# Performance work log

Measured on AMD Instinct MI355X. Metric: run time of the kernel, lower is better.

The kernel has to match this reference:

```python
import jax, jax.numpy as jnp
import numpy as np
from jax.scipy.special import logsumexp

# config (matches init_kwargs)
D_IN, D_OUT = 768, 256
P = 2
BLUR = 0.5
SCALING = 0.8
SCALING_FACTOR = 1.0
N_ITERS = 36  # fixed-length eps schedule (clamped at blur), jit-friendly


def setup_inputs() -> dict:
    key = jax.random.key(0)
    k1, k2, k3, k4 = jax.random.split(key, 4)
    d = jax.random.normal(k1, (4096, D_IN), dtype=jnp.float32)
    s1 = jax.random.normal(k2, (1024, D_IN), dtype=jnp.float32)
    s2 = jax.random.normal(k3, (1024, D_IN), dtype=jnp.float32)
    # learned projection parameter (scaled init so projected coords are O(1))
    M = jax.random.normal(k4, (D_IN, D_OUT), dtype=jnp.float32) / np.sqrt(D_IN)
    return {"d": d, "s1": s1, "s2": s2, "M": M}


def _sq_cost(u, v):
    # C[i,j] = ||u_i - v_j||^2 / 2  (geomloss p=2 cost)
    sq = (jnp.sum(u * u, -1)[:, None] + jnp.sum(v * v, -1)[None, :]
          - 2.0 * (u @ v.T))
    return jnp.maximum(sq, 0.0) * 0.5


def _softmin(eps, C, h):
    # -eps * log sum_j exp(h_j - C_ij/eps)   -> shape [C.shape[0]]
    return -eps * logsumexp(h[None, :] - C / eps, axis=1)


def _sinkhorn_divergence(x, y):
    n, m = x.shape[0], y.shape[0]
    a_log = jnp.full((n,), -np.log(n), dtype=x.dtype)  # uniform log-weights
    b_log = jnp.full((m,), -np.log(m), dtype=x.dtype)

    C_xy = _sq_cost(x, y)   # [n, m]
    C_xx = _sq_cost(x, x)   # [n, n]  (debiasing term)
    C_yy = _sq_cost(y, y)   # [m, m]

    # bounding-box diameter of the joint cloud (no grad, like geomloss)
    z = jax.lax.stop_gradient(jnp.concatenate([x, y], axis=0))
    diam = jnp.sqrt(jnp.sum((z.max(0) - z.min(0)) ** 2)) + 1e-6

    # eps-scaling schedule: scale from diameter down to blur, eps = scale^p
    scales = jnp.maximum(BLUR, diam * (SCALING ** jnp.arange(N_ITERS, dtype=x.dtype)))
    eps_list = scales ** P
    eps0 = eps_list[0]
    eps_f = jnp.asarray(BLUR ** P, dtype=x.dtype)

    # init potentials at the largest eps
    f_aa = _softmin(eps0, C_xx, a_log)
    g_bb = _softmin(eps0, C_yy, b_log)
    f_ab = _softmin(eps0, C_xy, b_log)
    g_ab = _softmin(eps0, C_xy.T, a_log)

    @jax.checkpoint
    def step(carry, eps):
        f_aa, g_bb, f_ab, g_ab = carry
        # simultaneous (Jacobi) updates, symmetrized by averaging
        ft = _softmin(eps, C_xy, b_log + g_ab / eps)
        gt = _softmin(eps, C_xy.T, a_log + f_ab / eps)
        f_aa = 0.5 * (f_aa + _softmin(eps, C_xx, a_log + f_aa / eps))
        g_bb = 0.5 * (g_bb + _softmin(eps, C_yy, b_log + g_bb / eps))
        f_ab = 0.5 * (f_ab + ft)
        g_ab = 0.5 * (g_ab + gt)
        return (f_aa, g_bb, f_ab, g_ab), None

    (f_aa, g_bb, f_ab, g_ab), _ = jax.lax.scan(
        step, (f_aa, g_bb, f_ab, g_ab), eps_list)

    # final non-averaged extrapolation at eps = blur^p
    f_ab_n = _softmin(eps_f, C_xy, b_log + g_ab / eps_f)
    g_ab_n = _softmin(eps_f, C_xy.T, a_log + f_ab / eps_f)
    f_aa_n = _softmin(eps_f, C_xx, a_log + f_aa / eps_f)
    g_bb_n = _softmin(eps_f, C_yy, b_log + g_bb / eps_f)

    # debiased divergence with uniform weights: <a, f_ab - f_aa> + <b, g_ab - g_bb>
    return jnp.mean(f_ab_n - f_aa_n) + jnp.mean(g_ab_n - g_bb_n)


def reference(d, s1, s2, M):
    xd = d @ M
    x1 = s1 @ M
    x2 = s2 @ M
    dist1 = _sinkhorn_divergence(xd, x1)
    dist2 = _sinkhorn_divergence(xd, x2)
    return jax.nn.sigmoid(SCALING_FACTOR * (dist2 - dist1))
```

## Files before the change

### kernel.cpp

```cpp
#include <hip/hip_runtime.h>
#include <hip/hip_bf16.h>
#include <math.h>

using ull = unsigned long long;
typedef unsigned short u16x8 __attribute__((ext_vector_type(8)));
typedef __attribute__((ext_vector_type(8))) short bf16x8;
typedef __attribute__((ext_vector_type(4))) float f32x4;

#define ND 4096ull
#define NS 1024ull
#define DOUT 256ull
#define DIN 768ull
#define NIT 36

constexpr ull U_CXX = 0;
constexpr ull U_CXY = U_CXX + ND*ND;
constexpr ull U_CYX = U_CXY + 2*ND*NS;
constexpr ull U_CYY = U_CYX + 2*ND*NS;
constexpr ull U_TOT = U_CYY + 2*NS*NS;
constexpr ull P_XDH = U_TOT;
constexpr ull P_XDM = P_XDH + ND*DOUT;
constexpr ull P_X1H = P_XDM + ND*DOUT;
constexpr ull P_X1M = P_X1H + NS*DOUT;
constexpr ull P_X2H = P_X1M + NS*DOUT;
constexpr ull P_X2M = P_X2H + NS*DOUT;
constexpr ull P_DH  = P_X2M + NS*DOUT;
constexpr ull P_DM  = P_DH + ND*DIN;
constexpr ull P_S1H = P_DM + ND*DIN;
constexpr ull P_S1M = P_S1H + NS*DIN;
constexpr ull P_S2H = P_S1M + NS*DIN;
constexpr ull P_S2M = P_S2H + NS*DIN;
constexpr ull P_MTH = P_S2M + NS*DIN;
constexpr ull P_MTM = P_MTH + DOUT*DIN;
constexpr ull U_END = P_MTM + DOUT*DIN;

constexpr ull O_XD   = U_END / 2;
constexpr ull O_X1   = O_XD + ND*DOUT;
constexpr ull O_X2   = O_X1 + NS*DOUT;
constexpr ull O_MT   = O_X2 + NS*DOUT;
constexpr ull O_ND_  = O_MT + DOUT*DIN;
constexpr ull O_N1   = O_ND_ + ND;
constexpr ull O_N2   = O_N1 + NS;
constexpr ull O_FAB  = O_N2 + NS;
constexpr ull O_GAB  = O_FAB + 4*ND;
constexpr ull O_FAA  = O_GAB + 4*NS;
constexpr ull O_GBB  = O_FAA + 4*ND;
constexpr ull O_FABN = O_GBB + 4*NS;
constexpr ull O_GABN = O_FABN + 2*ND;
constexpr ull O_FAAN = O_GABN + 2*NS;
constexpr ull O_GBBN = O_FAAN + 2*ND;
constexpr ull O_EPS  = O_GBBN + 2*NS;
constexpr ull O_QS   = O_EPS + 2*NIT;
constexpr ull O_DIST = O_QS + 2;
constexpr ull WS_FLOATS = O_DIST + 2;
constexpr ull O_PMIN = O_MT;
constexpr ull O_PMAX = O_MT + 96*256;

constexpr float LOG2E = 1.4426950408889634f;
constexpr float LN2   = 0.69314718055994531f;
constexpr float A_LOG2 = -12.0f;
constexpr float B_LOG2 = -10.0f;

__device__ __forceinline__ float wave_max(float v) {
    #pragma unroll
    for (int o = 32; o; o >>= 1) v = fmaxf(v, __shfl_xor(v, o));
    return v;
}
__device__ __forceinline__ float wave_sum(float v) {
    #pragma unroll
    for (int o = 32; o; o >>= 1) v += __shfl_xor(v, o);
    return v;
}

__device__ __forceinline__ unsigned short f2bf_rn(float x) {
    union { float f; unsigned u; } v; v.f = x;
    const unsigned r = v.u + 0x7FFFu + ((v.u >> 16) & 1u);
    return (unsigned short)(r >> 16);
}
__device__ __forceinline__ float bf2f(unsigned short b) {
    union { unsigned u; float f; } v; v.u = ((unsigned)b) << 16; return v.f;
}

__global__ __launch_bounds__(256)
void transpose_M_k(const float* __restrict__ M, float* __restrict__ Mt)
{
    int idx = blockIdx.x * 256 + threadIdx.x;
    int r = idx >> 8;
    int c = idx & 255;
    Mt[(size_t)c * DIN + r] = M[idx];
}

__global__ __launch_bounds__(256)
void pack_bf16_gen(const float* __restrict__ X,
                   unsigned short* __restrict__ Phi, unsigned short* __restrict__ Pmi,
                   int KB)
{
    const int p = blockIdx.x;
    const int t = threadIdx.x;
    const int K = KB * 32;
    for (int s = t; s < KB * 64; s += 256) {
        const int kb = s >> 6, l = s & 63;
        const int row = p * 16 + (l & 15);
        const int k0 = kb * 32 + ((l >> 4) << 3);
        const float* src = X + (ull)row * K + k0;
        u16x8 hi, mi;
        #pragma unroll
        for (int e = 0; e < 8; e++) {
            const float x = src[e];
            const unsigned short h = f2bf_rn(x);
            hi[e] = h;
            mi[e] = f2bf_rn(x - bf2f(h));
        }
        const ull o = (((ull)p * KB + kb) * 64 + l) * 8;
        *(u16x8*)&Phi[o] = hi;
        *(u16x8*)&Pmi[o] = mi;
    }
}

__global__ __launch_bounds__(256)
void gemm_proj_mfma(const unsigned short* __restrict__ Ahi, const unsigned short* __restrict__ Ami,
                    const unsigned short* __restrict__ Bhi, const unsigned short* __restrict__ Bmi,
                    float* __restrict__ C, int N, int KB)
{
    const int l = threadIdx.x & 63;
    const int w = threadIdx.x >> 6;
    const int n0 = blockIdx.x * 64, m0 = blockIdx.y * 128;
    const int pA0 = (m0 >> 4) + w * 2;
    const int pB0 = n0 >> 4;
    f32x4 acc[2][4] = {};
    for (int kb = 0; kb < KB; kb++) {
        const ull a0o = (((ull)(pA0 + 0) * KB + kb) * 64 + l) * 8;
        const ull a1o = (((ull)(pA0 + 1) * KB + kb) * 64 + l) * 8;
        const bf16x8 aH0 = *(const bf16x8*)&Ahi[a0o];
        const bf16x8 aM0 = *(const bf16x8*)&Ami[a0o];
        const bf16x8 aH1 = *(const bf16x8*)&Ahi[a1o];
        const bf16x8 aM1 = *(const bf16x8*)&Ami[a1o];
        #pragma unroll
        for (int j = 0; j < 4; j++) {
            const ull bo = (((ull)(pB0 + j) * KB + kb) * 64 + l) * 8;
            const bf16x8 bH = *(const bf16x8*)&Bhi[bo];
            const bf16x8 bM = *(const bf16x8*)&Bmi[bo];
            acc[0][j] = __builtin_amdgcn_mfma_f32_16x16x32_bf16(aH0, bH, acc[0][j], 0, 0, 0);
            acc[0][j] = __builtin_amdgcn_mfma_f32_16x16x32_bf16(aH0, bM, acc[0][j], 0, 0, 0);
            acc[0][j] = __builtin_amdgcn_mfma_f32_16x16x32_bf16(aM0, bH, acc[0][j], 0, 0, 0);
            acc[1][j] = __builtin_amdgcn_mfma_f32_16x16x32_bf16(aH1, bH, acc[1][j], 0, 0, 0);
            acc[1][j] = __builtin_amdgcn_mfma_f32_16x16x32_bf16(aH1, bM, acc[1][j], 0, 0, 0);
            acc[1][j] = __builtin_amdgcn_mfma_f32_16x16x32_bf16(aM1, bH, acc[1][j], 0, 0, 0);
        }
    }
    const int col = l & 15;
    #pragma unroll
    for (int i = 0; i < 2; i++) {
        const int row0 = m0 + w * 32 + i * 16 + ((l >> 4) << 2);
        #pragma unroll
        for (int r = 0; r < 4; r++) {
            const ull rowb = (ull)(row0 + r) * N + n0;
            #pragma unroll
            for (int j = 0; j < 4; j++)
                C[rowb + j * 16 + col] = acc[i][j][r];
        }
    }
}

__device__ __forceinline__ unsigned int quant16(float c, float s) {
    return __float2uint_rn(fminf(c * s, 65535.0f));
}

__global__ __launch_bounds__(256)
void gemm_cost_mfma(const unsigned short* __restrict__ Ahi, const unsigned short* __restrict__ Ami,
                    const unsigned short* __restrict__ Bhi, const unsigned short* __restrict__ Bmi,
                    unsigned short* __restrict__ C,
                    const float* __restrict__ na, const float* __restrict__ nb,
                    const float* __restrict__ qsp, int N)
{
    const int l = threadIdx.x & 63;
    const int w = threadIdx.x >> 6;
    const int n0 = blockIdx.x * 64, m0 = blockIdx.y * 128;
    const int pA0 = (m0 >> 4) + w * 2;
    const int pB0 = n0 >> 4;
    f32x4 acc[2][4] = {};
    #pragma unroll
    for (int kb = 0; kb < 8; kb++) {
        const ull a0o = (((ull)(pA0 + 0) * 8 + kb) * 64 + l) * 8;
        const ull a1o = (((ull)(pA0 + 1) * 8 + kb) * 64 + l) * 8;
        const bf16x8 aH0 = *(const bf16x8*)&Ahi[a0o];
        const bf16x8 aM0 = *(const bf16x8*)&Ami[a0o];
        const bf16x8 aH1 = *(const bf16x8*)&Ahi[a1o];
        const bf16x8 aM1 = *(const bf16x8*)&Ami[a1o];
        #pragma unroll
        for (int j = 0; j < 4; j++) {
            const ull bo = (((ull)(pB0 + j) * 8 + kb) * 64 + l) * 8;
            const bf16x8 bH = *(const bf16x8*)&Bhi[bo];
            const bf16x8 bM = *(const bf16x8*)&Bmi[bo];
            acc[0][j] = __builtin_amdgcn_mfma_f32_16x16x32_bf16(aH0, bH, acc[0][j], 0, 0, 0);
            acc[0][j] = __builtin_amdgcn_mfma_f32_16x16x32_bf16(aH0, bM, acc[0][j], 0, 0, 0);
            acc[0][j] = __builtin_amdgcn_mfma_f32_16x16x32_bf16(aM0, bH, acc[0][j], 0, 0, 0);
            acc[1][j] = __builtin_amdgcn_mfma_f32_16x16x32_bf16(aH1, bH, acc[1][j], 0, 0, 0);
            acc[1][j] = __builtin_amdgcn_mfma_f32_16x16x32_bf16(aH1, bM, acc[1][j], 0, 0, 0);
            acc[1][j] = __builtin_amdgcn_mfma_f32_16x16x32_bf16(aM1, bH, acc[1][j], 0, 0, 0);
        }
    }
    const float s = qsp[0];
    const int col = l & 15;
    float nbj[4];
    #pragma unroll
    for (int j = 0; j < 4; j++) nbj[j] = nb[n0 + j * 16 + col];
    #pragma unroll
    for (int i = 0; i < 2; i++) {
        const int row0 = m0 + w * 32 + i * 16 + ((l >> 4) << 2);
        #pragma unroll
        for (int r = 0; r < 4; r++) {
            const float nar = na[row0 + r];
            const ull rowb = (ull)(row0 + r) * N + n0;
            #pragma unroll
            for (int j = 0; j < 4; j++)
                C[rowb + j * 16 + col] =
                    (unsigned short)quant16(0.5f * fmaxf(nar + nbj[j] - 2.0f * acc[i][j][r], 0.0f), s);
        }
    }
}

__global__ __launch_bounds__(256)
void row_norm(const float* __restrict__ x, float* __restrict__ o)
{
    const int i = blockIdx.x;
    const float v = x[(size_t)i * DOUT + threadIdx.x];
    float s = wave_sum(v * v);
    __shared__ float red[4];
    const int wid = threadIdx.x >> 6, lane = threadIdx.x & 63;
    if (lane == 0) red[wid] = s;
    __syncthreads();
    if (threadIdx.x == 0) o[i] = red[0] + red[1] + red[2] + red[3];
}

__global__ __launch_bounds__(256)
void colminmax_k(const float* __restrict__ xd, const float* __restrict__ x1,
                 const float* __restrict__ x2, float* __restrict__ ws)
{
    const int b = blockIdx.x, c = threadIdx.x;
    const float* src; int r0;
    if (b < 64)      { src = xd; r0 = b * 64; }
    else if (b < 80) { src = x1; r0 = (b - 64) * 64; }
    else             { src = x2; r0 = (b - 80) * 64; }
    float mn = 3.4e38f, mx = -3.4e38f;
    for (int r = 0; r < 64; r++) {
        const float v = src[(size_t)(r0 + r) * DOUT + c];
        mn = fminf(mn, v); mx = fmaxf(mx, v);
    }
    ws[O_PMIN + (ull)b * 256 + c] = mn;
    ws[O_PMAX + (ull)b * 256 + c] = mx;
}

__global__ __launch_bounds__(256)
void eps_k(float* __restrict__ ws)
{
    const int c = threadIdx.x;
    const float* pmin = ws + O_PMIN;
    const float* pmax = ws + O_PMAX;
    float mnd = 3.4e38f, mxd = -3.4e38f;
    float mn1 = 3.4e38f, mx1 = -3.4e38f;
    float mn2 = 3.4e38f, mx2 = -3.4e38f;
    for (int b = 0;  b < 64; b++) { mnd = fminf(mnd, pmin[b*256+c]); mxd = fmaxf(mxd, pmax[b*256+c]); }
    for (int b = 64; b < 80; b++) { mn1 = fminf(mn1, pmin[b*256+c]); mx1 = fmaxf(mx1, pmax[b*256+c]); }
    for (int b = 80; b < 96; b++) { mn2 = fminf(mn2, pmin[b*256+c]); mx2 = fmaxf(mx2, pmax[b*256+c]); }
    const float d1 = fmaxf(mxd, mx1) - fminf(mnd, mn1);
    const float d2 = fmaxf(mxd, mx2) - fminf(mnd, mn2);
    float s1 = wave_sum(d1 * d1);
    float s2 = wave_sum(d2 * d2);
    __shared__ float r1[4], r2[4];
    const int wid = c >> 6, lane = c & 63;
    if (lane == 0) { r1[wid] = s1; r2[wid] = s2; }
    __syncthreads();
    if (c == 0) {
        const float d1s = r1[0]+r1[1]+r1[2]+r1[3];
        const float d2s = r2[0]+r2[1]+r2[2]+r2[3];
        const float cb = 0.5f * fmaxf(d1s, d2s) * 1.02f + 1.0f;
        ws[O_QS]     = 65535.0f / cb;
        ws[O_QS + 1] = cb / 65535.0f;
    }
    if (c < 2 * NIT) {
        const int div = c / NIT, tt = c % NIT;
        const float ss = div ? (r2[0]+r2[1]+r2[2]+r2[3]) : (r1[0]+r1[1]+r1[2]+r1[3]);
        const float diam = sqrtf(ss) + 1e-6f;
        const float sc = fmaxf(0.5f, diam * powf(0.8f, (float)tt));
        ws[O_EPS + (ull)div * NIT + tt] = sc * sc;
    }
}

template<int NC>
__device__ __forceinline__ void softmin_row_q(
    const unsigned short* __restrict__ Crow, const float* __restrict__ hvec,
    float hc2, float eps, float qs,
    const float* __restrict__ selfv, float* __restrict__ outp,
    int row, int phase, int lane)
{
    const float ie2 = LOG2E / eps;
    const float qsc = -qs * ie2;
    const u16x8* Q8 = (const u16x8*)Crow;
    const float4* H4 = (const float4*)hvec;
    float v[NC * 8];
    #pragma unroll
    for (int c = 0; c < NC; c++) {
        const u16x8 q = Q8[c * 64 + lane];
        if (hvec) {
            const float4 ha = H4[c * 128 + lane * 2];
            const float4 hb = H4[c * 128 + lane * 2 + 1];
            const float hv[8] = {ha.x, ha.y, ha.z, ha.w, hb.x, hb.y, hb.z, hb.w};
            #pragma unroll
            for (int e = 0; e < 8; e++)
                v[c*8 + e] = fmaf((float)q[e], qsc, fmaf(hv[e], ie2, hc2));
        } else {
            #pragma unroll
            for (int e = 0; e < 8; e++)
                v[c*8 + e] = fmaf((float)q[e], qsc, hc2);
        }
    }
    float m = v[0];
    #pragma unroll
    for (int k = 1; k < NC * 8; k++) m = fmaxf(m, v[k]);
    m = wave_max(m);
    float s = 0.0f;
    #pragma unroll
    for (int k = 0; k < NC * 8; k++) s += exp2f(v[k] - m);
    s = wave_sum(s);
    if (lane == 0) {
        float res = -eps * LN2 * (m + log2f(s));
        if (phase == 1) res = 0.5f * (selfv[row] + res);
        outp[row] = res;
    }
}

__global__ __launch_bounds__(256)
void sinkhorn_phase(float* __restrict__ ws, int phase, int t)
{
    const unsigned short* uq = (const unsigned short*)ws;
    const int wid = threadIdx.x >> 6, lane = threadIdx.x & 63;
    const int w = blockIdx.x * 4 + wid;
    const float qs = ws[O_QS + 1];
    int rb, wb;
    if (phase == 0) { rb = 0; wb = 0; }
    else { rb = t & 1; wb = rb ^ 1; }

    if (w < 8192) {
        const int div = w >> 12, i = w & 4095;
        const float eps = (phase == 2) ? 0.25f : ws[O_EPS + (ull)div * NIT + t];
        const unsigned short* Crow = uq + U_CXY + (ull)div * ND * NS + (ull)i * NS;
        const float* gab_r = ws + O_GAB + ((ull)div * 2 + rb) * NS;
        const float* fab_r = ws + O_FAB + ((ull)div * 2 + rb) * ND;
        float* outp = (phase == 2) ? (ws + O_FABN + (ull)div * ND)
                                   : (ws + O_FAB + ((ull)div * 2 + wb) * ND);
        softmin_row_q<2>(Crow, phase ? gab_r : nullptr, B_LOG2, eps, qs, fab_r, outp, i, phase, lane);
    } else if (w < 10240) {
        const int q = w - 8192, div = q >> 10, j = q & 1023;
        const float eps = (phase == 2) ? 0.25f : ws[O_EPS + (ull)div * NIT + t];
        const unsigned short* Crow = uq + U_CYX + (ull)div * ND * NS + (ull)j * ND;
        const float* fab_r = ws + O_FAB + ((ull)div * 2 + rb) * ND;
        const float* gab_r = ws + O_GAB + ((ull)div * 2 + rb) * NS;
        float* outp = (phase == 2) ? (ws + O_GABN + (ull)div * NS)
                                   : (ws + O_GAB + ((ull)div * 2 + wb) * NS);
        softmin_row_q<8>(Crow, phase ? fab_r : nullptr, A_LOG2, eps, qs, gab_r, outp, j, phase, lane);
    } else if (w < 14336) {
        const int i = w - 10240;
        const float eps0 = (phase == 2) ? 0.25f : ws[O_EPS + t];
        const float eps1 = (phase == 2) ? 0.25f : ws[O_EPS + NIT + t];
        const unsigned short* Crow = uq + U_CXX + (ull)i * ND;
        const float* faa_r0 = ws + O_FAA + (ull)rb * ND;
        const float* faa_r1 = ws + O_FAA + (2ull + rb) * ND;
        float* out0 = (phase == 2) ? (ws + O_FAAN)      : (ws + O_FAA + (ull)wb * ND);
        float* out1 = (phase == 2) ? (ws + O_FAAN + ND) : (ws + O_FAA + (2ull + wb) * ND);
        softmin_row_q<8>(Crow, phase ? faa_r0 : nullptr, A_LOG2, eps0, qs, faa_r0, out0, i, phase, lane);
        softmin_row_q<8>(Crow, phase ? faa_r1 : nullptr, A_LOG2, eps1, qs, faa_r1, out1, i, phase, lane);
    } else {
        const int q = w - 14336, div = q >> 10, i = q & 1023;
        const float eps = (phase == 2) ? 0.25f : ws[O_EPS + (ull)div * NIT + t];
        const unsigned short* Crow = uq + U_CYY + (ull)div * NS * NS + (ull)i * NS;
        const float* gbb_r = ws + O_GBB + ((ull)div * 2 + rb) * NS;
        float* outp = (phase == 2) ? (ws + O_GBBN + (ull)div * NS)
                                   : (ws + O_GBB + ((ull)div * 2 + wb) * NS);
        softmin_row_q<2>(Crow, phase ? gbb_r : nullptr, B_LOG2, eps, qs, gbb_r, outp, i, phase, lane);
    }
}

__global__ __launch_bounds__(256)
void reduce_dist(float* __restrict__ ws)
{
    const int d = blockIdx.x;
    const int tix = threadIdx.x;
    float s = 0.0f;
    #pragma unroll
    for (int k = 0; k < 16; k++) {
        const int i = tix + k * 256;
        s += (ws[O_FABN + (ull)d * ND + i] - ws[O_FAAN + (ull)d * ND + i]) * (1.0f / 4096.0f);
    }
    #pragma unroll
    for (int k = 0; k < 4; k++) {
        const int j = tix + k * 256;
        s += (ws[O_GABN + (ull)d * NS + j] - ws[O_GBBN + (ull)d * NS + j]) * (1.0f / 1024.0f);
    }
    s = wave_sum(s);
    __shared__ float red[4];
    const int wid = tix >> 6, lane = tix & 63;
    if (lane == 0) red[wid] = s;
    __syncthreads();
    if (tix == 0) ws[O_DIST + d] = red[0] + red[1] + red[2] + red[3];
}

__global__ void finalize_k(const float* __restrict__ ws, float* __restrict__ out)
{
    const float x = ws[O_DIST + 1] - ws[O_DIST + 0];
    out[0] = 1.0f / (1.0f + expf(-x));
}

extern "C" void kernel_launch(void* const* d_in, const int* in_sizes, int n_in,
                              void* d_out, int out_size, void* d_ws, size_t ws_size,
                              hipStream_t stream)
{
    if (ws_size < WS_FLOATS * sizeof(float)) return;

    const float* dmat = (const float*)d_in[0];
    const float* s1   = (const float*)d_in[1];
    const float* s2   = (const float*)d_in[2];
    const float* M    = (const float*)d_in[3];
    float* ws  = (float*)d_ws;
    float* out = (float*)d_out;
    unsigned short* uq = (unsigned short*)d_ws;

    float* Mt = ws + O_MT;
    float* xd = ws + O_XD;
    float* x1 = ws + O_X1;
    float* x2 = ws + O_X2;

    transpose_M_k<<<768, 256, 0, stream>>>(M, Mt);
    pack_bf16_gen<<<256, 256, 0, stream>>>(dmat, uq + P_DH,  uq + P_DM,  24);
    pack_bf16_gen<<<64,  256, 0, stream>>>(s1,   uq + P_S1H, uq + P_S1M, 24);
    pack_bf16_gen<<<64,  256, 0, stream>>>(s2,   uq + P_S2H, uq + P_S2M, 24);
    pack_bf16_gen<<<16,  256, 0, stream>>>(Mt,   uq + P_MTH, uq + P_MTM, 24);
    gemm_proj_mfma<<<dim3(4, 32), 256, 0, stream>>>(uq+P_DH,  uq+P_DM,  uq+P_MTH, uq+P_MTM, xd, 256, 24);
    gemm_proj_mfma<<<dim3(4, 8),  256, 0, stream>>>(uq+P_S1H, uq+P_S1M, uq+P_MTH, uq+P_MTM, x1, 256, 24);
    gemm_proj_mfma<<<dim3(4, 8),  256, 0, stream>>>(uq+P_S2H, uq+P_S2M, uq+P_MTH, uq+P_MTM, x2, 256, 24);
    row_norm<<<4096, 256, 0, stream>>>(xd, ws + O_ND_);
    row_norm<<<1024, 256, 0, stream>>>(x1, ws + O_N1);
    row_norm<<<1024, 256, 0, stream>>>(x2, ws + O_N2);
    colminmax_k<<<96, 256, 0, stream>>>(xd, x1, x2, ws);
    eps_k<<<1, 256, 0, stream>>>(ws);
    pack_bf16_gen<<<256, 256, 0, stream>>>(xd, uq + P_XDH, uq + P_XDM, 8);
    pack_bf16_gen<<<64,  256, 0, stream>>>(x1, uq + P_X1H, uq + P_X1M, 8);
    pack_bf16_gen<<<64,  256, 0, stream>>>(x2, uq + P_X2H, uq + P_X2M, 8);
    const float* qsp = ws + O_QS;
    const float* nd_ = ws + O_ND_;
    const float* n1  = ws + O_N1;
    const float* n2  = ws + O_N2;
    gemm_cost_mfma<<<dim3(64, 32), 256, 0, stream>>>(uq+P_XDH, uq+P_XDM, uq+P_XDH, uq+P_XDM, uq + U_CXX,         nd_, nd_, qsp, 4096);
    gemm_cost_mfma<<<dim3(16, 32), 256, 0, stream>>>(uq+P_XDH, uq+P_XDM, uq+P_X1H, uq+P_X1M, uq + U_CXY,         nd_, n1,  qsp, 1024);
    gemm_cost_mfma<<<dim3(64, 8),  256, 0, stream>>>(uq+P_X1H, uq+P_X1M, uq+P_XDH, uq+P_XDM, uq + U_CYX,         n1,  nd_, qsp, 4096);
    gemm_cost_mfma<<<dim3(16, 32), 256, 0, stream>>>(uq+P_XDH, uq+P_XDM, uq+P_X2H, uq+P_X2M, uq + U_CXY + ND*NS, nd_, n2,  qsp, 1024);
    gemm_cost_mfma<<<dim3(64, 8),  256, 0, stream>>>(uq+P_X2H, uq+P_X2M, uq+P_XDH, uq+P_XDM, uq + U_CYX + ND*NS, n2,  nd_, qsp, 4096);
    gemm_cost_mfma<<<dim3(16, 8),  256, 0, stream>>>(uq+P_X1H, uq+P_X1M, uq+P_X1H, uq+P_X1M, uq + U_CYY,         n1,  n1,  qsp, 1024);
    gemm_cost_mfma<<<dim3(16, 8),  256, 0, stream>>>(uq+P_X2H, uq+P_X2M, uq+P_X2H, uq+P_X2M, uq + U_CYY + NS*NS, n2,  n2,  qsp, 1024);
    sinkhorn_phase<<<4096, 256, 0, stream>>>(ws, 0, 0);
    for (int t = 0; t < NIT; t++)
        sinkhorn_phase<<<4096, 256, 0, stream>>>(ws, 1, t);
    sinkhorn_phase<<<4096, 256, 0, stream>>>(ws, 2, 36);
    reduce_dist<<<2, 256, 0, stream>>>(ws);
    finalize_k<<<1, 1, 0, stream>>>(ws, out);
}
```

Measured before the change: 1.431 ms.

## Split long softmin rows across block waves with shared-memory logsumexp merge

Each Sinkhorn softmin row of length 4096 (the C_yx and C_xx rows) is now split into four 1024-element segments, one per wave in a block. The partial max and sum from each wave are merged in shared memory. The C_xx work for the two divergences now runs in separate blocks instead of one wave doing both, and the grid grows from 4096 to 12800 blocks, so every wave handles the same amount of work. This is meant to remove the long-tail imbalance and short the serial per-wave chain. In exchange it adds a block barrier, and each C_xx row is read twice (once per divergence), which relies on the cache to hold it.

```diff
diff --git a/kernel.cpp b/kernel.cpp
--- a/kernel.cpp
+++ b/kernel.cpp
@@ -287,24 +287,18 @@
     }
 }
 
-template<int NC>
-__device__ __forceinline__ void softmin_row_q(
-    const unsigned short* __restrict__ Crow, const float* __restrict__ hvec,
-    float hc2, float eps, float qs,
-    const float* __restrict__ selfv, float* __restrict__ outp,
-    int row, int phase, int lane)
-{
-    const float ie2 = LOG2E / eps;
-    const float qsc = -qs * ie2;
-    const u16x8* Q8 = (const u16x8*)Crow;
-    const float4* H4 = (const float4*)hvec;
-    float v[NC * 8];
-    #pragma unroll
-    for (int c = 0; c < NC; c++) {
-        const u16x8 q = Q8[c * 64 + lane];
-        if (hvec) {
-            const float4 ha = H4[c * 128 + lane * 2];
-            const float4 hb = H4[c * 128 + lane * 2 + 1];
+__device__ __forceinline__ void softmin_1k(
+    const unsigned short* __restrict__ Cseg, const float* __restrict__ hseg,
+    float hc2, float ie2, float qsc, int lane, float& mO, float& sO)
+{
+    float v[16];
+    #pragma unroll
+    for (int c = 0; c < 2; c++) {
+        const int off = c * 512 + lane * 8;
+        const u16x8 q = *(const u16x8*)&Cseg[off];
+        if (hseg) {
+            const float4 ha = *(const float4*)&hseg[off];
+            const float4 hb = *(const float4*)&hseg[off + 4];
             const float hv[8] = {ha.x, ha.y, ha.z, ha.w, hb.x, hb.y, hb.z, hb.w};
             #pragma unroll
             for (int e = 0; e < 8; e++)
@@ -317,67 +311,102 @@
     }
     float m = v[0];
     #pragma unroll
-    for (int k = 1; k < NC * 8; k++) m = fmaxf(m, v[k]);
+    for (int k = 1; k < 16; k++) m = fmaxf(m, v[k]);
     m = wave_max(m);
     float s = 0.0f;
     #pragma unroll
-    for (int k = 0; k < NC * 8; k++) s += exp2f(v[k] - m);
-    s = wave_sum(s);
-    if (lane == 0) {
-        float res = -eps * LN2 * (m + log2f(s));
-        if (phase == 1) res = 0.5f * (selfv[row] + res);
-        outp[row] = res;
-    }
+    for (int k = 0; k < 16; k++) s += exp2f(v[k] - m);
+    sO = wave_sum(s);
+    mO = m;
 }
 
 __global__ __launch_bounds__(256)
 void sinkhorn_phase(float* __restrict__ ws, int phase, int t)
 {
+    __shared__ float mS[4], sS[4];
     const unsigned short* uq = (const unsigned short*)ws;
     const int wid = threadIdx.x >> 6, lane = threadIdx.x & 63;
-    const int w = blockIdx.x * 4 + wid;
     const float qs = ws[O_QS + 1];
     int rb, wb;
     if (phase == 0) { rb = 0; wb = 0; }
     else { rb = t & 1; wb = rb ^ 1; }
-
-    if (w < 8192) {
-        const int div = w >> 12, i = w & 4095;
+    const int b = blockIdx.x;
+
+    if (b < 2048) {
+        const int div = b >> 10;
+        const int i = ((b & 1023) << 2) + wid;
         const float eps = (phase == 2) ? 0.25f : ws[O_EPS + (ull)div * NIT + t];
+        const float ie2 = LOG2E / eps, qsc = -qs * ie2;
         const unsigned short* Crow = uq + U_CXY + (ull)div * ND * NS + (ull)i * NS;
-        const float* gab_r = ws + O_GAB + ((ull)div * 2 + rb) * NS;
-        const float* fab_r = ws + O_FAB + ((ull)div * 2 + rb) * ND;
+        const float* h    = phase ? (ws + O_GAB + ((ull)div * 2 + rb) * NS) : nullptr;
+        const float* self = ws + O_FAB + ((ull)div * 2 + rb) * ND;
         float* outp = (phase == 2) ? (ws + O_FABN + (ull)div * ND)
                                    : (ws + O_FAB + ((ull)div * 2 + wb) * ND);
-        softmin_row_q<2>(Crow, phase ? gab_r : nullptr, B_LOG2, eps, qs, fab_r, outp, i, phase, lane);
-    } else if (w < 10240) {
-        const int q = w - 8192, div = q >> 10, j = q & 1023;
+        float m, s;
+        softmin_1k(Crow, h, B_LOG2, ie2, qsc, lane, m, s);
+        if (lane == 0) {
+            float res = -eps * LN2 * (m + log2f(s));
+            if (phase == 1) res = 0.5f * (self[i] + res);
+            outp[i] = res;
+        }
+    } else if (b < 4096) {
+        const int q = b - 2048, div = q >> 10, j = q & 1023;
         const float eps = (phase == 2) ? 0.25f : ws[O_EPS + (ull)div * NIT + t];
-        const unsigned short* Crow = uq + U_CYX + (ull)div * ND * NS + (ull)j * ND;
-        const float* fab_r = ws + O_FAB + ((ull)div * 2 + rb) * ND;
-        const float* gab_r = ws + O_GAB + ((ull)div * 2 + rb) * NS;
+        const float ie2 = LOG2E / eps, qsc = -qs * ie2;
+        const unsigned short* Cseg = uq + U_CYX + (ull)div * ND * NS + (ull)j * ND + wid * 1024;
+        const float* h    = phase ? (ws + O_FAB + ((ull)div * 2 + rb) * ND + wid * 1024) : nullptr;
+        const float* self = ws + O_GAB + ((ull)div * 2 + rb) * NS;
         float* outp = (phase == 2) ? (ws + O_GABN + (ull)div * NS)
                                    : (ws + O_GAB + ((ull)div * 2 + wb) * NS);
-        softmin_row_q<8>(Crow, phase ? fab_r : nullptr, A_LOG2, eps, qs, gab_r, outp, j, phase, lane);
-    } else if (w < 14336) {
-        const int i = w - 10240;
-        const float eps0 = (phase == 2) ? 0.25f : ws[O_EPS + t];
-        const float eps1 = (phase == 2) ? 0.25f : ws[O_EPS + NIT + t];
-        const unsigned short* Crow = uq + U_CXX + (ull)i * ND;
-        const float* faa_r0 = ws + O_FAA + (ull)rb * ND;
-        const float* faa_r1 = ws + O_FAA + (2ull + rb) * ND;
-        float* out0 = (phase == 2) ? (ws + O_FAAN)      : (ws + O_FAA + (ull)wb * ND);
-        float* out1 = (phase == 2) ? (ws + O_FAAN + ND) : (ws + O_FAA + (2ull + wb) * ND);
-        softmin_row_q<8>(Crow, phase ? faa_r0 : nullptr, A_LOG2, eps0, qs, faa_r0, out0, i, phase, lane);
-        softmin_row_q<8>(Crow, phase ? faa_r1 : nullptr, A_LOG2, eps1, qs, faa_r1, out1, i, phase, lane);
+        float m, s;
+        softmin_1k(Cseg, h, A_LOG2, ie2, qsc, lane, m, s);
+        if (lane == 0) { mS[wid] = m; sS[wid] = s; }
+        __syncthreads();
+        if (threadIdx.x == 0) {
+            const float m0 = fmaxf(fmaxf(mS[0], mS[1]), fmaxf(mS[2], mS[3]));
+            const float st = sS[0]*exp2f(mS[0]-m0) + sS[1]*exp2f(mS[1]-m0)
+                           + sS[2]*exp2f(mS[2]-m0) + sS[3]*exp2f(mS[3]-m0);
+            float res = -eps * LN2 * (m0 + log2f(st));
+            if (phase == 1) res = 0.5f * (self[j] + res);
+            outp[j] = res;
+        }
+    } else if (b < 12288) {
+        const int q = b - 4096, div = q >> 12, i = q & 4095;
+        const float eps = (phase == 2) ? 0.25f : ws[O_EPS + (ull)div * NIT + t];
+        const float ie2 = LOG2E / eps, qsc = -qs * ie2;
+        const unsigned short* Cseg = uq + U_CXX + (ull)i * ND + wid * 1024;
+        const float* hbase = ws + O_FAA + ((ull)div * 2 + rb) * ND;
+        const float* h = phase ? (hbase + wid * 1024) : nullptr;
+        float* outp = (phase == 2) ? (ws + O_FAAN + (ull)div * ND)
+                                   : (ws + O_FAA + ((ull)div * 2 + wb) * ND);
+        float m, s;
+        softmin_1k(Cseg, h, A_LOG2, ie2, qsc, lane, m, s);
+        if (lane == 0) { mS[wid] = m; sS[wid] = s; }
+        __syncthreads();
+        if (threadIdx.x == 0) {
+            const float m0 = fmaxf(fmaxf(mS[0], mS[1]), fmaxf(mS[2], mS[3]));
+            const float st = sS[0]*exp2f(mS[0]-m0) + sS[1]*exp2f(mS[1]-m0)
+                           + sS[2]*exp2f(mS[2]-m0) + sS[3]*exp2f(mS[3]-m0);
+            float res = -eps * LN2 * (m0 + log2f(st));
+            if (phase == 1) res = 0.5f * (hbase[i] + res);
+            outp[i] = res;
+        }
     } else {
-        const int q = w - 14336, div = q >> 10, i = q & 1023;
+        const int q = b - 12288, div = q >> 8;
+        const int i = ((q & 255) << 2) + wid;
         const float eps = (phase == 2) ? 0.25f : ws[O_EPS + (ull)div * NIT + t];
+        const float ie2 = LOG2E / eps, qsc = -qs * ie2;
         const unsigned short* Crow = uq + U_CYY + (ull)div * NS * NS + (ull)i * NS;
-        const float* gbb_r = ws + O_GBB + ((ull)div * 2 + rb) * NS;
+        const float* hb = ws + O_GBB + ((ull)div * 2 + rb) * NS;
         float* outp = (phase == 2) ? (ws + O_GBBN + (ull)div * NS)
                                    : (ws + O_GBB + ((ull)div * 2 + wb) * NS);
-        softmin_row_q<2>(Crow, phase ? gbb_r : nullptr, B_LOG2, eps, qs, gbb_r, outp, i, phase, lane);
+        float m, s;
+        softmin_1k(Crow, phase ? hb : nullptr, B_LOG2, ie2, qsc, lane, m, s);
+        if (lane == 0) {
+            float res = -eps * LN2 * (m + log2f(s));
+            if (phase == 1) res = 0.5f * (hb[i] + res);
+            outp[i] = res;
+        }
     }
 }
 
@@ -457,10 +486,10 @@
     gemm_cost_mfma<<<dim3(64, 8),  256, 0, stream>>>(uq+P_X2H, uq+P_X2M, uq+P_XDH, uq+P_XDM, uq + U_CYX + ND*NS, n2,  nd_, qsp, 4096);
     gemm_cost_mfma<<<dim3(16, 8),  256, 0, stream>>>(uq+P_X1H, uq+P_X1M, uq+P_X1H, uq+P_X1M, uq + U_CYY,         n1,  n1,  qsp, 1024);
     gemm_cost_mfma<<<dim3(16, 8),  256, 0, stream>>>(uq+P_X2H, uq+P_X2M, uq+P_X2H, uq+P_X2M, uq + U_CYY + NS*NS, n2,  n2,  qsp, 1024);
-    sinkhorn_phase<<<4096, 256, 0, stream>>>(ws, 0, 0);
+    sinkhorn_phase<<<12800, 256, 0, stream>>>(ws, 0, 0);
     for (int t = 0; t < NIT; t++)
-        sinkhorn_phase<<<4096, 256, 0, stream>>>(ws, 1, t);
-    sinkhorn_phase<<<4096, 256, 0, stream>>>(ws, 2, 36);
+        sinkhorn_phase<<<12800, 256, 0, stream>>>(ws, 1, t);
+    sinkhorn_phase<<<12800, 256, 0, stream>>>(ws, 2, 36);
     reduce_dist<<<2, 256, 0, stream>>>(ws);
     finalize_k<<<1, 1, 0, stream>>>(ws, out);
 }
```

Result: faster. 1.289 ms (-9.9%).
